# Kernel optimization log

Hardware: AMD Instinct MI355X
Metric: run time of the kernel (lower is better)

## Reference

```python
import jax, jax.numpy as jnp
import numpy as np
import math
from jax import lax

S = 2048   # layer_size (number of neurons)
T = 384    # timesteps per forward call
ALPHA = 0.15
DT = 0.1
THRESH = -50.0
V_RESET = -70.0
VL = -70.0
GL = 0.025
CM = 0.5
TAU = CM / GL                                   # 20.0
COEF = DT ** ALPHA * math.gamma(2.0 - ALPHA) / CM  # dt^alpha * Gamma(2-alpha) / Cm


def setup_inputs() -> dict:
    key = jax.random.key(0)
    I_old = jax.random.normal(key, (S, T), dtype=jnp.float32)
    # class-level fractional (Grunwald-Letnikov style) weight vector, x=5000
    x = 5000
    nv = np.arange(x - 1)
    w = ((x - nv + 1) ** (1.0 - ALPHA) - (x - nv) ** (1.0 - ALPHA)).astype(np.float32)
    return {"I_old": I_old, "weights": jnp.asarray(w)}


def _forward(I_old, weights):
    S_, T_ = I_old.shape
    dtype = I_old.dtype
    # wr[a] = weights[-a]: the memory weight applied to a delta that is `a` steps old.
    # Original: np.inner(weights[-N+1:], delta_trace) pairs oldest delta with weights[-(N-1)]
    # and the newest delta with weights[-1].
    wr = jnp.concatenate([jnp.zeros((1,), dtype), weights[::-1][:T_].astype(dtype)])  # [T+1]
    jidx = jnp.arange(T_)  # buffer slot j holds the delta appended at global step j

    def step(carry, xs):
        V, buf = carry          # V: [S], buf: [S, T] delta history (slot j = delta of step j)
        n, I_n = xs             # n: scalar step index, I_n: [S]
        # fractional memory term: sum_{j=1}^{n-1} wr[n-j] * delta_j
        ages = n - jidx                                        # [T]
        coeff = jnp.where((ages >= 1) & (jidx >= 1),
                          wr[jnp.clip(ages, 0, T_)], jnp.zeros((), dtype))  # [T]
        memory = buf @ coeff                                   # [S]
        # three update rules depending on the global step counter
        V1 = V + (DT / TAU) * (-V + I_n / GL)                  # N == 1 branch
        V2 = COEF * (-GL * (V - VL) + I_n) + V - memory        # N >= 2 branch
        V_pre = jnp.where(n == 0, jnp.full_like(V, -70.0),
                          jnp.where(n == 1, V1, V2))
        spike = (V - THRESH > 0).astype(dtype)                 # spike uses PREVIOUS V
        reset = lax.stop_gradient(spike * (THRESH - V_RESET))  # detached reset
        V_new = V_pre - reset
        buf = buf.at[:, n].set(V_new - V)                      # append delta (n=0 slot masked out)
        return (V_new, buf), (spike, V_new)

    V0 = jnp.zeros((S_,), dtype)          # V_trace initialized to 0 per neuron
    buf0 = jnp.zeros((S_, T_), dtype)
    (_, _), (spk, trc) = lax.scan(step, (V0, buf0), (jnp.arange(T_), I_old.T))
    return spk.T, trc.T                    # each [S, T]


def reference(I_old, weights):
    return _forward(I_old, weights)
```

## Files before the change

kernel.cpp:

```cpp
#include <hip/hip_runtime.h>
#include <cmath>

#define T_STEPS 384
#define CH 64
#define NCH 6
#define WS 392

__device__ __forceinline__ float readlane_f(float v, int l) {
    return __int_as_float(__builtin_amdgcn_readlane(__float_as_int(v), l));
}
__device__ __forceinline__ float wave_shr1_f(float v) {
    return __int_as_float(__builtin_amdgcn_mov_dpp(__float_as_int(v), 0x138, 0xf, 0xf, true));
}

__global__ __launch_bounds__(128, 4)
void flif_kernel(const float* __restrict__ I_old, const float* __restrict__ W,
                 float* __restrict__ out, float cm1, float c2, float c3, int Stot)
{
    const int tid  = threadIdx.x;
    const int wid  = tid >> 6;
    const int lane = tid & 63;
    const int s    = blockIdx.x;

    __shared__ __align__(16) float wtr[4 * WS];
    __shared__ __align__(16) float dbuf[T_STEPS];
    __shared__ float accs[2][CH];

    for (int k = tid; k < 4 * WS; k += 128) {
        const int r = k / WS, kk = k - r * WS;
        const int i = kk + r;
        wtr[k] = (i <= 382) ? W[4998 - i] : 0.0f;
    }
    ((float*)accs)[tid] = 0.0f;
    __syncthreads();

    const int rl = lane & 3;
    const float* wlp = wtr + rl * WS + (lane - rl);

    if (wid == 1) {
        float A2 = 0.0f, A3 = 0.0f, A4 = 0.0f, A5 = 0.0f;
        #pragma unroll
        for (int c = 0; c < NCH; ++c) {
            if (c >= 1 && c <= 4) {
                const int src = c - 1;
                const float* dp = dbuf + src * CH;
                #pragma unroll
                for (int k = 0; k <= 60; k += 4) {
                    const float4 d4 = *reinterpret_cast<const float4*>(dp + k);
                    #pragma unroll
                    for (int t = c + 1; t <= 5; ++t) {
                        const int g = t - src;
                        const float4 w4 = *reinterpret_cast<const float4*>(wlp + (g * 64 - k - 4));
                        float& At = (t == 2) ? A2 : (t == 3) ? A3 : (t == 4) ? A4 : A5;
                        At = fmaf(d4.x, w4.w, At);
                        At = fmaf(d4.y, w4.z, At);
                        At = fmaf(d4.z, w4.y, At);
                        At = fmaf(d4.w, w4.x, At);
                    }
                }
                const float hand = (c == 1) ? A2 : (c == 2) ? A3 : (c == 3) ? A4 : A5;
                accs[(c + 1) & 1][lane] = hand;
            }
            __syncthreads();
        }
        return;
    }

    const float* Irow = I_old + (size_t)s * T_STEPS;
    float Inext = Irow[lane];
    const float w0seed = (lane >= 1) ? W[4999 - lane] : 0.0f;
    const float wr1n = -W[4998];
    const float b1 = cm1 - W[4998];
    const float b2 = cm1 - W[4997];
    const float w2seed = (lane >= 1) ? (cm1 - W[4999 - lane]) : 0.0f;

    float Vcs = 0.0f;
    float rvprev = 0.0f;
    float tcs[NCH], spks[NCH];

    for (int c = 0; c < NCH; ++c) {
        const int cb = c * CH;
        const float Ic = Inext;
        if (c + 1 < NCH) Inext = Irow[cb + CH + lane];

        float acc = (c == 0) ? 0.0f : accs[c & 1][lane];
        if (c >= 1) {
            const float* dp = dbuf + (c - 1) * CH;
            #pragma unroll
            for (int m0 = 60; m0 >= 0; m0 -= 4) {
                const float4 d4 = *reinterpret_cast<const float4*>(dp + (60 - m0));
                const float4 w4 = *reinterpret_cast<const float4*>(wlp + m0);
                acc = fmaf(d4.x, w4.w, acc);
                acc = fmaf(d4.y, w4.z, acc);
                acc = fmaf(d4.z, w4.y, acc);
                acc = fmaf(d4.w, w4.x, acc);
            }
        }

        const float u0 = fmaf(c3, Ic, c2) - acc;
        const float Vs = Vcs;
        float tc = 0.0f;
        float Vend;

        {
            float u, S, Pq0, Pq1, w2;
            float dm1 = 0.0f, dm2 = 0.0f;
            if (c == 0) {
                float V0 = -90.0f;
                if (lane == 0) tc = V0;
                const float wf = wave_shr1_f(w0seed);
                const float I1 = readlane_f(Ic, 1);
                const float V1 = fmaf(0.005f, (I1 / 0.025f) - V0, V0);
                const float d1 = V1 - V0;
                const float ue = fmaf(-wf, d1, u0);
                if (lane == 1) tc = V1;
                u = fmaf(cm1, V1, ue);
                S = V1;
                Pq0 = readlane_f(u, 2);
                Pq1 = readlane_f(u, 3);
                w2 = wave_shr1_f(wave_shr1_f(w2seed));
                #pragma unroll
                for (int i = 2; i < CH; ++i) {
                    const float x  = fmaf(b2, dm2, (i & 1) ? Pq1 : Pq0);
                    const float dn = fmaf(b1, dm1, x);
                    const float nf = readlane_f(u, (i + 2) & 63);
                    if (i & 1) Pq1 = nf; else Pq0 = nf;
                    u = fmaf(w2, dn, u);
                    w2 = wave_shr1_f(w2);
                    S += dn;
                    tc = (lane == i) ? S : tc;
                    dm2 = dm1; dm1 = dn;
                }
                Vend = S;
            } else {
                u = fmaf(cm1, Vcs, u0);
                S = 0.0f;
                Pq0 = readlane_f(u, 0) + rvprev;
                Pq1 = readlane_f(u, 1);
                w2 = w2seed;
                #pragma unroll
                for (int i = 0; i < CH; ++i) {
                    const float x  = fmaf(b2, dm2, (i & 1) ? Pq1 : Pq0);
                    const float dn = fmaf(b1, dm1, x);
                    const float nf = readlane_f(u, (i + 2) & 63);
                    if (i & 1) Pq1 = nf; else Pq0 = nf;
                    u = fmaf(w2, dn, u);
                    w2 = wave_shr1_f(w2);
                    S += dn;
                    tc = (lane == i) ? S : tc;
                    dm2 = dm1; dm1 = dn;
                }
                tc = Vcs + tc;
                Vend = Vcs + S;
            }
        }

        if (__any(tc > -50.5f)) {
            float V, d, b, P, w;
            float tcf = 0.0f;
            float uf = u0;
            if (c == 0) {
                V = -90.0f;
                if (lane == 0) tcf = V;
                w = wave_shr1_f(w0seed);
                const float I1 = readlane_f(Ic, 1);
                const float V1 = fmaf(0.005f, (I1 / 0.025f) - V, V);
                const float d1 = V1 - V;
                P = readlane_f(uf, 2);
                uf = fmaf(-w, d1, uf);
                w = wave_shr1_f(w);
                if (lane == 1) tcf = V1;
                V = V1; d = d1;
                b = fmaf(cm1, V, (V > -50.0f) ? -20.0f : 0.0f);
                #pragma unroll
                for (int i = 2; i < CH; ++i) {
                    const float t = fmaf(wr1n, d, P);
                    d = t + b;
                    P = readlane_f(uf, (i + 1) & 63);
                    V = V + d;
                    const float rv = (V > -50.0f) ? -20.0f : 0.0f;
                    b = fmaf(cm1, V, rv);
                    uf = fmaf(-w, d, uf);
                    w = wave_shr1_f(w);
                    tcf = (lane == i) ? V : tcf;
                }
            } else {
                V = Vcs; d = 0.0f;
                b = fmaf(cm1, Vcs, rvprev);
                w = w0seed;
                P = readlane_f(uf, 0);
                #pragma unroll
                for (int i = 0; i < CH; ++i) {
                    const float t = fmaf(wr1n, d, P);
                    d = t + b;
                    P = readlane_f(uf, (i + 1) & 63);
                    V = V + d;
                    const float rv = (V > -50.0f) ? -20.0f : 0.0f;
                    b = fmaf(cm1, V, rv);
                    uf = fmaf(-w, d, uf);
                    w = wave_shr1_f(w);
                    tcf = (lane == i) ? V : tcf;
                }
            }
            tc = tcf; Vend = V;
        }
        rvprev = (Vend > -50.0f) ? -20.0f : 0.0f;

        float prev = __shfl_up(tc, 1);
        if (lane == 0) prev = Vs;
        spks[c] = (prev > -50.0f) ? 1.0f : 0.0f;
        float dd = tc - prev;
        if (c == 0 && lane == 0) dd = 0.0f;
        dbuf[cb + lane] = dd;
        tcs[c] = tc;
        Vcs = Vend;
        __syncthreads();
    }

    float* out_spk = out + (size_t)s * T_STEPS;
    float* out_trc = out + (size_t)Stot * T_STEPS + (size_t)s * T_STEPS;
    #pragma unroll
    for (int c = 0; c < NCH; ++c) {
        out_spk[c * CH + lane] = spks[c];
        out_trc[c * CH + lane] = tcs[c];
    }
}

extern "C" void kernel_launch(void* const* d_in, const int* in_sizes, int n_in,
                              void* d_out, int out_size, void* d_ws, size_t ws_size,
                              hipStream_t stream) {
    const float* I = (const float*)d_in[0];
    const float* W = (const float*)d_in[1];
    float* out = (float*)d_out;
    const int S = in_sizes[0] / T_STEPS;

    const double COEF = std::pow(0.1, 0.15) * std::tgamma(1.85) / 0.5;
    const float c3  = (float)COEF;
    const float cm1 = (float)(-COEF * 0.025);
    const float c2  = (float)(COEF * 0.025 * -70.0);

    flif_kernel<<<S, 128, 0, stream>>>(I, W, out, cm1, c2, c3, S);
}
```

Measured before the change: 75.93 us.

## Replace serial running sums with DPP wave scan and packed FMAs

Inside the serial 64-step recurrence, the per-lane running sum and lane-select of the trace are dropped. Each step's delta is written to shared memory, and the trace is then rebuilt with a DPP inclusive prefix-sum across the wave. The convolution dot products now use two-wide packed FMA accumulators, and the weight table is stored with adjacent pairs swapped so it lines up with those packed lanes. The goal is a shorter dependency chain in the critical loop, at the cost of extra LDS stores, a reordered floating-point summation, and a replay path that rewrites dbuf only when it is taken.

```diff
diff --git a/kernel.cpp b/kernel.cpp
--- a/kernel.cpp
+++ b/kernel.cpp
@@ -6,11 +6,27 @@
 #define NCH 6
 #define WS 392
 
+typedef float v2f __attribute__((ext_vector_type(2)));
+typedef float v4f __attribute__((ext_vector_type(4)));
+
 __device__ __forceinline__ float readlane_f(float v, int l) {
     return __int_as_float(__builtin_amdgcn_readlane(__float_as_int(v), l));
 }
 __device__ __forceinline__ float wave_shr1_f(float v) {
     return __int_as_float(__builtin_amdgcn_mov_dpp(__float_as_int(v), 0x138, 0xf, 0xf, true));
+}
+template<int CTRL, int RM>
+__device__ __forceinline__ float dpp0_f(float v) {
+    return __int_as_float(__builtin_amdgcn_update_dpp(0, __float_as_int(v), CTRL, RM, 0xf, true));
+}
+__device__ __forceinline__ float wave_iscan_add(float v) {
+    v += dpp0_f<0x111, 0xf>(v);
+    v += dpp0_f<0x112, 0xf>(v);
+    v += dpp0_f<0x114, 0xf>(v);
+    v += dpp0_f<0x118, 0xf>(v);
+    v += dpp0_f<0x142, 0xa>(v);
+    v += dpp0_f<0x143, 0xc>(v);
+    return v;
 }
 
 __global__ __launch_bounds__(128, 4)
@@ -28,7 +44,7 @@
 
     for (int k = tid; k < 4 * WS; k += 128) {
         const int r = k / WS, kk = k - r * WS;
-        const int i = kk + r;
+        const int i = (kk ^ 1) + r;
         wtr[k] = (i <= 382) ? W[4998 - i] : 0.0f;
     }
     ((float*)accs)[tid] = 0.0f;
@@ -38,7 +54,7 @@
     const float* wlp = wtr + rl * WS + (lane - rl);
 
     if (wid == 1) {
-        float A2 = 0.0f, A3 = 0.0f, A4 = 0.0f, A5 = 0.0f;
+        v2f A2 = {0.0f, 0.0f}, A3 = {0.0f, 0.0f}, A4 = {0.0f, 0.0f}, A5 = {0.0f, 0.0f};
         #pragma unroll
         for (int c = 0; c < NCH; ++c) {
             if (c >= 1 && c <= 4) {
@@ -46,20 +62,18 @@
                 const float* dp = dbuf + src * CH;
                 #pragma unroll
                 for (int k = 0; k <= 60; k += 4) {
-                    const float4 d4 = *reinterpret_cast<const float4*>(dp + k);
+                    const v4f d4 = *reinterpret_cast<const v4f*>(dp + k);
                     #pragma unroll
                     for (int t = c + 1; t <= 5; ++t) {
                         const int g = t - src;
-                        const float4 w4 = *reinterpret_cast<const float4*>(wlp + (g * 64 - k - 4));
-                        float& At = (t == 2) ? A2 : (t == 3) ? A3 : (t == 4) ? A4 : A5;
-                        At = fmaf(d4.x, w4.w, At);
-                        At = fmaf(d4.y, w4.z, At);
-                        At = fmaf(d4.z, w4.y, At);
-                        At = fmaf(d4.w, w4.x, At);
+                        const v4f w4 = *reinterpret_cast<const v4f*>(wlp + (g * 64 - k - 4));
+                        v2f& At = (t == 2) ? A2 : (t == 3) ? A3 : (t == 4) ? A4 : A5;
+                        At = d4.xy * w4.zw + At;
+                        At = d4.zw * w4.xy + At;
                     }
                 }
-                const float hand = (c == 1) ? A2 : (c == 2) ? A3 : (c == 3) ? A4 : A5;
-                accs[(c + 1) & 1][lane] = hand;
+                const v2f hv = (c == 1) ? A2 : (c == 2) ? A3 : (c == 3) ? A4 : A5;
+                accs[(c + 1) & 1][lane] = hv.x + hv.y;
             }
             __syncthreads();
         }
@@ -86,36 +100,35 @@
         float acc = (c == 0) ? 0.0f : accs[c & 1][lane];
         if (c >= 1) {
             const float* dp = dbuf + (c - 1) * CH;
+            v2f a2 = {0.0f, 0.0f};
             #pragma unroll
             for (int m0 = 60; m0 >= 0; m0 -= 4) {
-                const float4 d4 = *reinterpret_cast<const float4*>(dp + (60 - m0));
-                const float4 w4 = *reinterpret_cast<const float4*>(wlp + m0);
-                acc = fmaf(d4.x, w4.w, acc);
-                acc = fmaf(d4.y, w4.z, acc);
-                acc = fmaf(d4.z, w4.y, acc);
-                acc = fmaf(d4.w, w4.x, acc);
-            }
+                const v4f d4 = *reinterpret_cast<const v4f*>(dp + (60 - m0));
+                const v4f w4 = *reinterpret_cast<const v4f*>(wlp + m0);
+                a2 = d4.xy * w4.zw + a2;
+                a2 = d4.zw * w4.xy + a2;
+            }
+            acc += a2.x + a2.y;
         }
 
         const float u0 = fmaf(c3, Ic, c2) - acc;
         const float Vs = Vcs;
-        float tc = 0.0f;
+        float tc;
         float Vend;
 
         {
-            float u, S, Pq0, Pq1, w2;
+            float u, Pq0, Pq1, w2;
             float dm1 = 0.0f, dm2 = 0.0f;
             if (c == 0) {
-                float V0 = -90.0f;
-                if (lane == 0) tc = V0;
+                const float V0 = -90.0f;
                 const float wf = wave_shr1_f(w0seed);
                 const float I1 = readlane_f(Ic, 1);
                 const float V1 = fmaf(0.005f, (I1 / 0.025f) - V0, V0);
                 const float d1 = V1 - V0;
                 const float ue = fmaf(-wf, d1, u0);
-                if (lane == 1) tc = V1;
                 u = fmaf(cm1, V1, ue);
-                S = V1;
+                dbuf[0] = 0.0f;
+                dbuf[1] = d1;
                 Pq0 = readlane_f(u, 2);
                 Pq1 = readlane_f(u, 3);
                 w2 = wave_shr1_f(wave_shr1_f(w2seed));
@@ -127,14 +140,14 @@
                     if (i & 1) Pq1 = nf; else Pq0 = nf;
                     u = fmaf(w2, dn, u);
                     w2 = wave_shr1_f(w2);
-                    S += dn;
-                    tc = (lane == i) ? S : tc;
+                    dbuf[i] = dn;
                     dm2 = dm1; dm1 = dn;
                 }
-                Vend = S;
+                const float dl = dbuf[lane];
+                tc = -90.0f + wave_iscan_add(dl);
+                Vend = readlane_f(tc, 63);
             } else {
                 u = fmaf(cm1, Vcs, u0);
-                S = 0.0f;
                 Pq0 = readlane_f(u, 0) + rvprev;
                 Pq1 = readlane_f(u, 1);
                 w2 = w2seed;
@@ -146,16 +159,18 @@
                     if (i & 1) Pq1 = nf; else Pq0 = nf;
                     u = fmaf(w2, dn, u);
                     w2 = wave_shr1_f(w2);
-                    S += dn;
-                    tc = (lane == i) ? S : tc;
+                    dbuf[cb + i] = dn;
                     dm2 = dm1; dm1 = dn;
                 }
-                tc = Vcs + tc;
-                Vend = Vcs + S;
-            }
-        }
-
+                const float dl = dbuf[cb + lane];
+                tc = Vcs + wave_iscan_add(dl);
+                Vend = readlane_f(tc, 63);
+            }
+        }
+
+        bool replayed = false;
         if (__any(tc > -50.5f)) {
+            replayed = true;
             float V, d, b, P, w;
             float tcf = 0.0f;
             float uf = u0;
@@ -209,9 +224,11 @@
         float prev = __shfl_up(tc, 1);
         if (lane == 0) prev = Vs;
         spks[c] = (prev > -50.0f) ? 1.0f : 0.0f;
-        float dd = tc - prev;
-        if (c == 0 && lane == 0) dd = 0.0f;
-        dbuf[cb + lane] = dd;
+        if (replayed) {
+            float dd = tc - prev;
+            if (c == 0 && lane == 0) dd = 0.0f;
+            dbuf[cb + lane] = dd;
+        }
         tcs[c] = tc;
         Vcs = Vend;
         __syncthreads();
```

Measured after the change: 75.53 us. Within noise of the previous version (-0.5%).
